# Kernel optimization log

Measured on AMD Instinct MI355X. Metric: run time of the kernel, lower is better.

The kernel has to match this reference:

```python
import jax, jax.numpy as jnp
import numpy as np

N = 50000          # points
K = 16             # neighbors per query (n_max)
M = N * K          # ragged pair count
DIM = 96
HEADS = 6
HEAD_DIM = DIM // HEADS
WINDOW = 4.0
QUANT = 0.25
QGL = int(WINDOW / QUANT)   # quant_grid_length = 16
SCALE = HEAD_DIM ** -0.5


def setup_inputs() -> dict:
    key = jax.random.key(0)
    ks = jax.random.split(key, 10)
    feats = jax.random.normal(ks[0], (N, DIM), dtype=jnp.float32)
    xyz = jax.random.uniform(ks[1], (N, 3), dtype=jnp.float32) * 8.0
    index_0 = jnp.repeat(jnp.arange(N, dtype=jnp.int32), K)            # sorted query ids
    index_1 = jax.random.randint(ks[2], (M,), 0, N, dtype=jnp.int32)   # neighbor ids
    index_0_offsets = jnp.arange(N + 1, dtype=jnp.int32) * K
    W_qkv = jax.random.normal(ks[3], (DIM, 3 * DIM), dtype=jnp.float32) * 0.02
    b_qkv = jnp.zeros((3 * DIM,), dtype=jnp.float32)
    table_q = jax.random.normal(ks[4], (4 * QGL, HEADS, HEAD_DIM, 3), dtype=jnp.float32) * 0.02
    table_k = jax.random.normal(ks[5], (4 * QGL, HEADS, HEAD_DIM, 3), dtype=jnp.float32) * 0.02
    table_v = jax.random.normal(ks[6], (4 * QGL, HEADS, HEAD_DIM, 3), dtype=jnp.float32) * 0.02
    W_proj = jax.random.normal(ks[7], (DIM, DIM), dtype=jnp.float32) * 0.02
    b_proj = jnp.zeros((DIM,), dtype=jnp.float32)
    return {
        "feats": feats, "xyz": xyz,
        "index_0": index_0, "index_0_offsets": index_0_offsets, "n_max": K,
        "index_1": index_1, "shift_size": jnp.float32(0.0),
        "W_qkv": W_qkv, "b_qkv": b_qkv,
        "table_q": table_q, "table_k": table_k, "table_v": table_v,
        "W_proj": W_proj, "b_proj": b_proj,
    }


def reference(feats, xyz, index_0, index_0_offsets, n_max, index_1, shift_size,
              W_qkv, b_qkv, table_q, table_k, table_v, W_proj, b_proj):
    n = feats.shape[0]
    # qkv projection -> (N, 3, H, HD)
    qkv = (feats @ W_qkv + b_qkv).reshape(n, 3, HEADS, HEAD_DIM)
    q = qkv[:, 0] * SCALE
    k = qkv[:, 1]
    v = qkv[:, 2]

    # step1: per-pair QK dot product (pointops.attention_step1_v2)
    qg = q[index_0]                      # (M, H, HD) gathered by query id
    kg = k[index_1]                      # (M, H, HD) gathered by neighbor id
    attn = jnp.einsum('mhd,mhd->mh', qg, kg)   # (M, H)

    # quantized relative positions
    xyz_quant = jnp.floor(((xyz - xyz.min(axis=0) + shift_size) % WINDOW) / QUANT)
    rel = xyz_quant[index_0] - xyz_quant[index_1]       # (M, 3)
    rel_idx = (rel + (QGL - 1)).astype(jnp.int32)       # map_func, in [0, 2*QGL-2]

    # relative position bias (pointops.dot_prod_with_idx_v3: query + key tables)
    bias = jnp.zeros_like(attn)
    for c in range(3):   # fixed 3 coordinate axes
        tq = table_q[rel_idx[:, c], :, :, c]            # (M, H, HD)
        tk = table_k[rel_idx[:, c], :, :, c]
        bias = bias + jnp.einsum('mhd,mhd->mh', qg, tq) + jnp.einsum('mhd,mhd->mh', kg, tk)
    attn = attn + bias

    # scatter softmax over index_0 segments
    seg_max = jax.ops.segment_max(attn, index_0, num_segments=n)
    e = jnp.exp(attn - seg_max[index_0])
    denom = jax.ops.segment_sum(e, index_0, num_segments=n)
    sm = e / denom[index_0]                              # (M, H)

    # step2 with relative position value (pointops.attention_step2_with_rel_pos_value_v2)
    vg = v[index_1]                                      # (M, H, HD)
    for c in range(3):
        vg = vg + table_v[rel_idx[:, c], :, :, c]
    x = jax.ops.segment_sum(sm[:, :, None] * vg, index_0, num_segments=n)  # (N, H, HD)
    x = x.reshape(n, DIM)
    return x @ W_proj + b_proj
```

## Files before the change

### kernel.cpp

```cpp
#include <hip/hip_runtime.h>
#include <hip/hip_fp16.h>
#include <math.h>

#define FLT_BIG 3.402823466e38f
typedef unsigned int uint;
typedef unsigned short ushort;
typedef __attribute__((ext_vector_type(8))) _Float16 half8;
typedef __attribute__((ext_vector_type(4))) float floatx4;

__device__ inline ushort f2h(float f) {
    return __half_as_ushort(__float2half(f));
}
__device__ inline float dot2(uint a, uint b, float c) {
    float d;
    asm("v_dot2_f32_f16 %0, %1, %2, %3" : "=v"(d) : "v"(a), "v"(b), "v"(c));
    return d;
}
template <int CTRL>
__device__ inline float dppf(float x) {
    return __int_as_float(__builtin_amdgcn_update_dpp(
        __float_as_int(x), __float_as_int(x), CTRL, 0xF, 0xF, true));
}

__global__ void prep_min_kernel(const float* __restrict__ W_qkv,
                                const float* __restrict__ W_proj,
                                const float* __restrict__ tq, const float* __restrict__ tk,
                                const float* __restrict__ tv,
                                const float* __restrict__ xyz,
                                ushort* __restrict__ wtqkv, ushort* __restrict__ wtproj,
                                ushort* __restrict__ rq, ushort* __restrict__ rk,
                                ushort* __restrict__ rv, float* mn, int n) {
    int tid = blockIdx.x * 256 + threadIdx.x;
    if (tid < 18432) {
        int c = tid / 6144, rem = tid - c * 6144;
        int idx = rem / 96, hd = rem - idx * 96;
        int src = (idx * 96 + hd) * 3 + c;
        rq[tid] = f2h(tq[src]);
        rk[tid] = f2h(tk[src]);
        rv[tid] = f2h(tv[src]);
    }
    if (tid < 27648) {
        int j = tid / 96, d = tid - j * 96;
        wtqkv[tid] = f2h(W_qkv[d * 288 + j]);
    }
    if (tid < 9216) {
        int j = tid / 96, d = tid - j * 96;
        wtproj[tid] = f2h(W_proj[d * 96 + j]);
    }
    float m0 = FLT_BIG, m1 = FLT_BIG, m2 = FLT_BIG;
    for (int i = tid; i < n; i += gridDim.x * 256) {
        m0 = fminf(m0, xyz[3 * i + 0]);
        m1 = fminf(m1, xyz[3 * i + 1]);
        m2 = fminf(m2, xyz[3 * i + 2]);
    }
#pragma unroll
    for (int off = 32; off > 0; off >>= 1) {
        m0 = fminf(m0, __shfl_down(m0, off));
        m1 = fminf(m1, __shfl_down(m1, off));
        m2 = fminf(m2, __shfl_down(m2, off));
    }
    if ((threadIdx.x & 63) == 0) {
        atomicMin((int*)&mn[0], __float_as_int(m0));
        atomicMin((int*)&mn[1], __float_as_int(m1));
        atomicMin((int*)&mn[2], __float_as_int(m2));
    }
}

__global__ __launch_bounds__(384) void qkv_mfma_kernel(
    const float* __restrict__ A, const ushort* __restrict__ WT,
    const float* __restrict__ bias, uint4* __restrict__ qout4,
    uint4* __restrict__ kvout4, const float* __restrict__ xyz,
    const float* __restrict__ mn, const float* __restrict__ shiftp,
    uint* __restrict__ xq, int n) {
    __shared__ ushort Ash[64 * 104];
    __shared__ ushort lds[6][32 * 112];
    const int t = threadIdx.x;
    const int row0 = blockIdx.x * 64;

    if (t < 64) {
        int rp = row0 + t;
        if (rp < n) {
            float shift = shiftp[0];
            float q0 = floorf(fmodf(xyz[3 * rp + 0] - mn[0] + shift, 4.0f) * 4.0f);
            float q1 = floorf(fmodf(xyz[3 * rp + 1] - mn[1] + shift, 4.0f) * 4.0f);
            float q2 = floorf(fmodf(xyz[3 * rp + 2] - mn[2] + shift, 4.0f) * 4.0f);
            xq[rp] = (uint)(int)q0 | ((uint)(int)q1 << 8) | ((uint)(int)q2 << 16);
        }
    }

    const float4* A4 = (const float4*)A;
#pragma unroll
    for (int j = 0; j < 4; j++) {
        int idx = t + j * 384;
        int row = idx / 24, c4 = idx - row * 24;
        int gr = row0 + row; if (gr > n - 1) gr = n - 1;
        float4 v = A4[(size_t)gr * 24 + c4];
        uint2 pk;
        pk.x = (uint)f2h(v.x) | ((uint)f2h(v.y) << 16);
        pk.y = (uint)f2h(v.z) | ((uint)f2h(v.w) << 16);
        *(uint2*)&Ash[row * 104 + c4 * 4] = pk;
    }
    __syncthreads();

    const int wave = t >> 6, lane = t & 63;
    const int ch = wave >> 1, rg = wave & 1;
    const int m = lane & 15, q = lane >> 4;
    const int wrow0 = row0 + rg * 32;

    const ushort* wbase = WT + ((size_t)ch * 96 + m) * 96 + q * 8;

    floatx4 acc[2][6];
#pragma unroll
    for (int g = 0; g < 2; g++)
#pragma unroll
        for (int ct = 0; ct < 6; ct++) acc[g][ct] = (floatx4){0.f, 0.f, 0.f, 0.f};

#pragma unroll
    for (int kk4 = 0; kk4 < 24; kk4 += 8) {
        half8 a0 = *(const half8*)&Ash[(rg * 32 + m) * 104 + (kk4 + q * 2) * 4];
        half8 a1 = *(const half8*)&Ash[(rg * 32 + 16 + m) * 104 + (kk4 + q * 2) * 4];
#pragma unroll
        for (int ct = 0; ct < 6; ct++) {
            half8 b = *(const half8*)(wbase + ct * 16 * 96 + kk4 * 4);
            acc[0][ct] = __builtin_amdgcn_mfma_f32_16x16x32_f16(a0, b, acc[0][ct], 0, 0, 0);
            acc[1][ct] = __builtin_amdgcn_mfma_f32_16x16x32_f16(a1, b, acc[1][ct], 0, 0, 0);
        }
    }

    ushort* L = lds[wave];
    const float sc = (ch == 0) ? 0.25f : 1.0f;
#pragma unroll
    for (int g = 0; g < 2; g++)
#pragma unroll
        for (int ct = 0; ct < 6; ct++) {
            float bv = bias[ch * 96 + ct * 16 + m];
#pragma unroll
            for (int r = 0; r < 4; r++) {
                int rowl = g * 16 + q * 4 + r;
                L[rowl * 112 + ct * 16 + m] = f2h((acc[g][ct][r] + bv) * sc);
            }
        }
    const int strideU4 = (ch == 0) ? 12 : 24;
    const int offU4 = (ch == 2) ? 12 : 0;
    uint4* dst = (ch == 0) ? qout4 : kvout4;
#pragma unroll
    for (int i = 0; i < 6; i++) {
        int idx = i * 64 + lane;
        int rowl = idx / 12, u4 = idx - rowl * 12;
        int grow = wrow0 + rowl;
        if (grow < n) {
            uint4 val = *(const uint4*)(L + rowl * 112 + u4 * 8);
            dst[(size_t)grow * strideU4 + offU4 + u4] = val;
        }
    }
}

#define ATTN_NB 256
#define ATTN_B 8
#define QPITCH 208
#define VPITCH 192
#define KOFF 39936
#define VOFF 79872
#define XOFF 116736
#define XPITCH 104
__global__ __launch_bounds__(768) void attn_proj_kernel(
    const ushort* __restrict__ qh, const ushort* __restrict__ kv,
    const uint* __restrict__ xq, const int* __restrict__ index_1,
    const ushort* __restrict__ rq, const ushort* __restrict__ rk,
    const ushort* __restrict__ rv, const ushort* __restrict__ wtproj,
    const float* __restrict__ b_proj, float* __restrict__ out, int n) {
    __shared__ __align__(16) char Lb[158336];

    const int t = threadIdx.x, b = blockIdx.x;
    const int pt = t / 96, tp = t - pt * 96;
    const int h = tp >> 4, e = tp & 15;

    const int stride = ATTN_NB * ATTN_B;
    const int iters = (n + stride - 1) / stride;

    int pA, jdA; uint xqpA;
    auto PREF_A = [&](int it) {
        pA = (it * ATTN_NB + b) * ATTN_B + pt;
        int pc = pA < n ? pA : n - 1;
        jdA = index_1[(size_t)pc * 16 + e];
        xqpA = xq[pc];
    };
    int p, jd; uint xqp, xqj;
    uint4 ka, kb, va, vb, qa, qb;
    auto PREF_B = [&]() {
        p = pA; jd = jdA; xqp = xqpA;
        int pc = p < n ? p : n - 1;
        const ushort* row = kv + (size_t)jd * 192;
        ka = *(const uint4*)(row + h * 16);
        kb = *(const uint4*)(row + h * 16 + 8);
        va = *(const uint4*)(row + 96 + h * 16);
        vb = *(const uint4*)(row + 96 + h * 16 + 8);
        const ushort* qrow = qh + (size_t)pc * 96 + h * 16;
        qa = *(const uint4*)qrow;
        qb = *(const uint4*)(qrow + 8);
        xqj = xq[jd];
    };
    PREF_A(0); PREF_B(); PREF_A(1);

#pragma unroll
    for (int j = 0; j < 9; j++) {
        const int tbl = j / 3;
        const uint4* src = (tbl == 0) ? (const uint4*)rq
                         : (tbl == 1) ? (const uint4*)rk : (const uint4*)rv;
        int rem = t + (j % 3) * 768;
        int ROW = rem / 12, slot = rem - ROW * 12;
        uint4 val = src[rem];
        const int base = (tbl == 0) ? 0 : (tbl == 1) ? KOFF : VOFF;
        const int pitch = (tbl == 2) ? VPITCH : QPITCH;
        *(uint4*)(Lb + base + ROW * pitch + slot * 16) = val;
    }
    __syncthreads();

    auto LD2Q = [&](const char* base, int R, uint4& A, uint4& B) {
        const char* rb = base + R * QPITCH + h * 32;
        A = *(const uint4*)rb;
        B = *(const uint4*)(rb + 16);
    };
    auto F2 = [](const uint4& u, int i) -> float2 {
        return __half22float2(((const __half2*)&u)[i]);
    };

    const bool b3 = (e & 8) != 0, b2 = (e & 4) != 0;
    const bool b1 = (e & 2) != 0, b0 = (e & 1) != 0;

    for (int it = 0; it < iters; it++) {
        const int i0 = (int)(xqp & 255u) - (int)(xqj & 255u) + 15;
        const int i1 = (int)((xqp >> 8) & 255u) - (int)((xqj >> 8) & 255u) + 15;
        const int i2 = (int)((xqp >> 16) & 255u) - (int)((xqj >> 16) & 255u) + 15;

        float f[16];
#pragma unroll
        for (int i = 0; i < 4; i++) {
            float2 lo = F2(va, i), hi = F2(vb, i);
            f[2 * i] = lo.x; f[2 * i + 1] = lo.y;
            f[8 + 2 * i] = hi.x; f[8 + 2 * i + 1] = hi.y;
        }

        float a;
        {
            float x0 = dot2(qa.x, ka.x, 0.f), x1 = dot2(qa.y, ka.y, 0.f);
            x0 = dot2(qa.z, ka.z, x0); x1 = dot2(qa.w, ka.w, x1);
            x0 = dot2(qb.x, kb.x, x0); x1 = dot2(qb.y, kb.y, x1);
            x0 = dot2(qb.z, kb.z, x0); x1 = dot2(qb.w, kb.w, x1);
            float bias = 0.f;
#define BIAS_C(ROW)                                                            \
            {                                                                  \
                uint4 ta, tb, ua, ub;                                          \
                LD2Q(Lb, (ROW), ta, tb);                                       \
                LD2Q(Lb + KOFF, (ROW), ua, ub);                                \
                float u = dot2(qa.x, ta.x, 0.f), w = dot2(ka.x, ua.x, 0.f);    \
                u = dot2(qa.y, ta.y, u); w = dot2(ka.y, ua.y, w);              \
                u = dot2(qa.z, ta.z, u); w = dot2(ka.z, ua.z, w);              \
                u = dot2(qa.w, ta.w, u); w = dot2(ka.w, ua.w, w);              \
                u = dot2(qb.x, tb.x, u); w = dot2(kb.x, ub.x, w);              \
                u = dot2(qb.y, tb.y, u); w = dot2(kb.y, ub.y, w);              \
                u = dot2(qb.z, tb.z, u); w = dot2(kb.z, ub.z, w);              \
                u = dot2(qb.w, tb.w, u); w = dot2(kb.w, ub.w, w);              \
                bias += u + w;                                                 \
            }
            BIAS_C(i0)
            BIAS_C(64 + i1)
            BIAS_C(128 + i2)
#undef BIAS_C
            a = x0 + x1 + bias;
        }

        if (it + 1 < iters) { PREF_B(); PREF_A(it + 2); }

        {
            uint4 t0a, t0b, t1a, t1b, t2a, t2b;
            {
                const char* rb = Lb + VOFF + i0 * VPITCH + h * 32;
                t0a = *(const uint4*)rb; t0b = *(const uint4*)(rb + 16);
            }
            {
                const char* rb = Lb + VOFF + (64 + i1) * VPITCH + h * 32;
                t1a = *(const uint4*)rb; t1b = *(const uint4*)(rb + 16);
            }
            {
                const char* rb = Lb + VOFF + (128 + i2) * VPITCH + h * 32;
                t2a = *(const uint4*)rb; t2b = *(const uint4*)(rb + 16);
            }
#pragma unroll
            for (int i = 0; i < 4; i++) {
                float2 a0 = F2(t0a, i), a1 = F2(t1a, i), a2 = F2(t2a, i);
                f[2 * i]     += a0.x + a1.x + a2.x;
                f[2 * i + 1] += a0.y + a1.y + a2.y;
                float2 c0 = F2(t0b, i), c1 = F2(t1b, i), c2 = F2(t2b, i);
                f[8 + 2 * i]     += c0.x + c1.x + c2.x;
                f[8 + 2 * i + 1] += c0.y + c1.y + c2.y;
            }
        }

        float wgt;
        {
            float mx = a;
            mx = fmaxf(mx, dppf<0x128>(mx));
            mx = fmaxf(mx, dppf<0x124>(mx));
            mx = fmaxf(mx, dppf<0x122>(mx));
            mx = fmaxf(mx, dppf<0x121>(mx));
            float ex = __expf(a - mx);
            float sum = ex;
            sum += dppf<0x128>(sum);
            sum += dppf<0x124>(sum);
            sum += dppf<0x122>(sum);
            sum += dppf<0x121>(sum);
            wgt = ex * __builtin_amdgcn_rcpf(sum);
        }

        float P[16];
#pragma unroll
        for (int c = 0; c < 16; c++) P[c] = wgt * f[c];
        float A8[8];
#pragma unroll
        for (int j = 0; j < 8; j++) {
            float kp = b3 ? P[j + 8] : P[j];
            float sd = b3 ? P[j] : P[j + 8];
            A8[j] = kp + dppf<0x140>(sd);
        }
        float B4[4];
#pragma unroll
        for (int j = 0; j < 4; j++) {
            float kp = b2 ? A8[j + 4] : A8[j];
            float sd = b2 ? A8[j] : A8[j + 4];
            B4[j] = kp + dppf<0x141>(sd);
        }
        float C2[2];
#pragma unroll
        for (int j = 0; j < 2; j++) {
            float kp = b1 ? B4[j + 2] : B4[j];
            float sd = b1 ? B4[j] : B4[j + 2];
            C2[j] = kp + dppf<0x4E>(sd);
        }
        {
            float kp = b0 ? C2[1] : C2[0];
            float sd = b0 ? C2[0] : C2[1];
            float xres = kp + dppf<0xB1>(sd);
            *(ushort*)(Lb + XOFF + (it * ATTN_B + pt) * (XPITCH * 2) + tp * 2) =
                f2h(xres);
        }
    }
    __syncthreads();

    {
        const int wave = t >> 6, lane = t & 63;
        const int m = lane & 15, q = lane >> 4;
        const int row0l = wave * 32;
        const int nloc = iters * ATTN_B;
        if (row0l < nloc) {
            const ushort* X = (const ushort*)(Lb + XOFF);
            const ushort* wbase = wtproj + (size_t)m * 96 + q * 8;
            int r0 = row0l + m;      if (r0 > nloc - 1) r0 = nloc - 1;
            int r1 = row0l + 16 + m; if (r1 > nloc - 1) r1 = nloc - 1;
            floatx4 acc[2][6];
#pragma unroll
            for (int g = 0; g < 2; g++)
#pragma unroll
                for (int ct = 0; ct < 6; ct++) acc[g][ct] = (floatx4){0.f, 0.f, 0.f, 0.f};
#pragma unroll
            for (int kk = 0; kk < 96; kk += 32) {
                half8 a0 = *(const half8*)(X + r0 * XPITCH + q * 8 + kk);
                half8 a1 = *(const half8*)(X + r1 * XPITCH + q * 8 + kk);
#pragma unroll
                for (int ct = 0; ct < 6; ct++) {
                    half8 bb = *(const half8*)(wbase + ct * 16 * 96 + kk);
                    acc[0][ct] = __builtin_amdgcn_mfma_f32_16x16x32_f16(a0, bb, acc[0][ct], 0, 0, 0);
                    acc[1][ct] = __builtin_amdgcn_mfma_f32_16x16x32_f16(a1, bb, acc[1][ct], 0, 0, 0);
                }
            }
#pragma unroll
            for (int g = 0; g < 2; g++)
#pragma unroll
                for (int ct = 0; ct < 6; ct++) {
                    int col = ct * 16 + m;
                    float bv = b_proj[col];
#pragma unroll
                    for (int r = 0; r < 4; r++) {
                        int lr = row0l + g * 16 + q * 4 + r;
                        if (lr < nloc) {
                            int grow = (lr >> 3) * stride + b * ATTN_B + (lr & 7);
                            if (grow < n)
                                out[(size_t)grow * 96 + col] = acc[g][ct][r] + bv;
                        }
                    }
                }
        }
    }
}

extern "C" void kernel_launch(void* const* d_in, const int* in_sizes, int n_in,
                              void* d_out, int out_size, void* d_ws, size_t ws_size,
                              hipStream_t stream) {
    const float* feats   = (const float*)d_in[0];
    const float* xyz     = (const float*)d_in[1];
    const int*   index_1 = (const int*)d_in[5];
    const float* shiftp  = (const float*)d_in[6];
    const float* W_qkv   = (const float*)d_in[7];
    const float* b_qkv   = (const float*)d_in[8];
    const float* table_q = (const float*)d_in[9];
    const float* table_k = (const float*)d_in[10];
    const float* table_v = (const float*)d_in[11];
    const float* W_proj  = (const float*)d_in[12];
    const float* b_proj  = (const float*)d_in[13];
    float* out = (float*)d_out;

    const int n = in_sizes[0] / 96;

    float* w = (float*)d_ws;
    float*  mn     = w;
    ushort* qbf    = (ushort*)(w + 16);
    ushort* kvbuf  = qbf + (size_t)n * 96;
    ushort* wtqkv  = kvbuf + (size_t)n * 192;
    ushort* wtproj = wtqkv + 27648;
    ushort* rq     = wtproj + 9216;
    ushort* rk     = rq + 18432;
    ushort* rv     = rk + 18432;
    uint*   xqv    = (uint*)(rv + 18432);

    hipMemsetAsync(mn, 0x7F, 3 * sizeof(float), stream);
    prep_min_kernel<<<108, 256, 0, stream>>>(W_qkv, W_proj, table_q, table_k,
                                             table_v, xyz, wtqkv, wtproj,
                                             rq, rk, rv, mn, n);
    qkv_mfma_kernel<<<(n + 63) / 64, 384, 0, stream>>>(feats, wtqkv, b_qkv,
                                                       (uint4*)qbf, (uint4*)kvbuf,
                                                       xyz, mn, shiftp, xqv, n);
    attn_proj_kernel<<<ATTN_NB, 768, 0, stream>>>(qbf, kvbuf, xqv, index_1,
                                                  rq, rk, rv, wtproj, b_proj,
                                                  out, n);
}
```

Measured before the change: 200.7 us.

## Process two points per thread-group per iteration and sum value tables in half2

Each 96-thread group now handles two query points per loop iteration (16 points per block iteration instead of 8), doubling the number of independent gathers and computations in flight per thread. This is meant to expose more memory-level and instruction-level parallelism to hide gather latency, with half the iterations. The three relative-position value table rows are also summed in packed fp16 before conversion, which cuts conversion and add work but loses a little precision. The cost is higher register pressure, and the shared X buffer grows with more rows per block.

```diff
diff --git a/kernel.cpp b/kernel.cpp
--- a/kernel.cpp
+++ b/kernel.cpp
@@ -156,51 +156,52 @@
 }
 
 #define ATTN_NB 256
-#define ATTN_B 8
+#define PPB 16
 #define QPITCH 208
 #define VPITCH 192
 #define KOFF 39936
 #define VOFF 79872
 #define XOFF 116736
 #define XPITCH 104
-__global__ __launch_bounds__(768) void attn_proj_kernel(
+__global__ __launch_bounds__(768, 3) void attn_proj_kernel(
     const ushort* __restrict__ qh, const ushort* __restrict__ kv,
     const uint* __restrict__ xq, const int* __restrict__ index_1,
     const ushort* __restrict__ rq, const ushort* __restrict__ rk,
     const ushort* __restrict__ rv, const ushort* __restrict__ wtproj,
     const float* __restrict__ b_proj, float* __restrict__ out, int n) {
-    __shared__ __align__(16) char Lb[158336];
+    __shared__ __align__(16) char Lb[160000];
 
     const int t = threadIdx.x, b = blockIdx.x;
     const int pt = t / 96, tp = t - pt * 96;
     const int h = tp >> 4, e = tp & 15;
 
-    const int stride = ATTN_NB * ATTN_B;
+    const int stride = ATTN_NB * PPB;
     const int iters = (n + stride - 1) / stride;
 
-    int pA, jdA; uint xqpA;
-    auto PREF_A = [&](int it) {
-        pA = (it * ATTN_NB + b) * ATTN_B + pt;
-        int pc = pA < n ? pA : n - 1;
-        jdA = index_1[(size_t)pc * 16 + e];
-        xqpA = xq[pc];
+    int pA[2], jdA[2]; uint xqpA[2];
+    auto PREF_A = [&](int it, int u) {
+        pA[u] = (it * ATTN_NB + b) * PPB + u * 8 + pt;
+        int pc = pA[u] < n ? pA[u] : n - 1;
+        jdA[u] = index_1[(size_t)pc * 16 + e];
+        xqpA[u] = xq[pc];
     };
-    int p, jd; uint xqp, xqj;
-    uint4 ka, kb, va, vb, qa, qb;
-    auto PREF_B = [&]() {
-        p = pA; jd = jdA; xqp = xqpA;
-        int pc = p < n ? p : n - 1;
-        const ushort* row = kv + (size_t)jd * 192;
-        ka = *(const uint4*)(row + h * 16);
-        kb = *(const uint4*)(row + h * 16 + 8);
-        va = *(const uint4*)(row + 96 + h * 16);
-        vb = *(const uint4*)(row + 96 + h * 16 + 8);
+    int p[2], jd[2]; uint xqp[2], xqj[2];
+    uint4 ka[2], kb[2], va[2], vb[2], qa[2], qb[2];
+    auto PREF_B = [&](int u) {
+        p[u] = pA[u]; jd[u] = jdA[u]; xqp[u] = xqpA[u];
+        int pc = p[u] < n ? p[u] : n - 1;
+        const ushort* row = kv + (size_t)jd[u] * 192;
+        ka[u] = *(const uint4*)(row + h * 16);
+        kb[u] = *(const uint4*)(row + h * 16 + 8);
+        va[u] = *(const uint4*)(row + 96 + h * 16);
+        vb[u] = *(const uint4*)(row + 96 + h * 16 + 8);
         const ushort* qrow = qh + (size_t)pc * 96 + h * 16;
-        qa = *(const uint4*)qrow;
-        qb = *(const uint4*)(qrow + 8);
-        xqj = xq[jd];
+        qa[u] = *(const uint4*)qrow;
+        qb[u] = *(const uint4*)(qrow + 8);
+        xqj[u] = xq[jd[u]];
     };
-    PREF_A(0); PREF_B(); PREF_A(1);
+    PREF_A(0, 0); PREF_A(0, 1); PREF_B(0); PREF_B(1);
+    PREF_A(1, 0); PREF_A(1, 1);
 
 #pragma unroll
     for (int j = 0; j < 9; j++) {
@@ -224,125 +225,146 @@
     auto F2 = [](const uint4& u, int i) -> float2 {
         return __half22float2(((const __half2*)&u)[i]);
     };
-
-    const bool b3 = (e & 8) != 0, b2 = (e & 4) != 0;
-    const bool b1 = (e & 2) != 0, b0 = (e & 1) != 0;
+    auto H2 = [](const uint4& u, int i) -> __half2 {
+        return ((const __half2*)&u)[i];
+    };
+
+    const bool e3 = (e & 8) != 0, e2 = (e & 4) != 0;
+    const bool e1 = (e & 2) != 0, e0 = (e & 1) != 0;
 
     for (int it = 0; it < iters; it++) {
-        const int i0 = (int)(xqp & 255u) - (int)(xqj & 255u) + 15;
-        const int i1 = (int)((xqp >> 8) & 255u) - (int)((xqj >> 8) & 255u) + 15;
-        const int i2 = (int)((xqp >> 16) & 255u) - (int)((xqj >> 16) & 255u) + 15;
-
-        float f[16];
-#pragma unroll
-        for (int i = 0; i < 4; i++) {
-            float2 lo = F2(va, i), hi = F2(vb, i);
-            f[2 * i] = lo.x; f[2 * i + 1] = lo.y;
-            f[8 + 2 * i] = hi.x; f[8 + 2 * i + 1] = hi.y;
-        }
-
-        float a;
-        {
-            float x0 = dot2(qa.x, ka.x, 0.f), x1 = dot2(qa.y, ka.y, 0.f);
-            x0 = dot2(qa.z, ka.z, x0); x1 = dot2(qa.w, ka.w, x1);
-            x0 = dot2(qb.x, kb.x, x0); x1 = dot2(qb.y, kb.y, x1);
-            x0 = dot2(qb.z, kb.z, x0); x1 = dot2(qb.w, kb.w, x1);
+        int i0[2], i1[2], i2[2];
+#pragma unroll
+        for (int u = 0; u < 2; u++) {
+            i0[u] = (int)(xqp[u] & 255u) - (int)(xqj[u] & 255u) + 15;
+            i1[u] = (int)((xqp[u] >> 8) & 255u) - (int)((xqj[u] >> 8) & 255u) + 15;
+            i2[u] = (int)((xqp[u] >> 16) & 255u) - (int)((xqj[u] >> 16) & 255u) + 15;
+        }
+
+        float f[2][16];
+#pragma unroll
+        for (int u = 0; u < 2; u++)
+#pragma unroll
+            for (int i = 0; i < 4; i++) {
+                float2 lo = F2(va[u], i), hi = F2(vb[u], i);
+                f[u][2 * i] = lo.x; f[u][2 * i + 1] = lo.y;
+                f[u][8 + 2 * i] = hi.x; f[u][8 + 2 * i + 1] = hi.y;
+            }
+
+        float a[2];
+#pragma unroll
+        for (int u = 0; u < 2; u++) {
+            float x0 = dot2(qa[u].x, ka[u].x, 0.f), x1 = dot2(qa[u].y, ka[u].y, 0.f);
+            x0 = dot2(qa[u].z, ka[u].z, x0); x1 = dot2(qa[u].w, ka[u].w, x1);
+            x0 = dot2(qb[u].x, kb[u].x, x0); x1 = dot2(qb[u].y, kb[u].y, x1);
+            x0 = dot2(qb[u].z, kb[u].z, x0); x1 = dot2(qb[u].w, kb[u].w, x1);
             float bias = 0.f;
 #define BIAS_C(ROW)                                                            \
             {                                                                  \
                 uint4 ta, tb, ua, ub;                                          \
                 LD2Q(Lb, (ROW), ta, tb);                                       \
                 LD2Q(Lb + KOFF, (ROW), ua, ub);                                \
-                float u = dot2(qa.x, ta.x, 0.f), w = dot2(ka.x, ua.x, 0.f);    \
-                u = dot2(qa.y, ta.y, u); w = dot2(ka.y, ua.y, w);              \
-                u = dot2(qa.z, ta.z, u); w = dot2(ka.z, ua.z, w);              \
-                u = dot2(qa.w, ta.w, u); w = dot2(ka.w, ua.w, w);              \
-                u = dot2(qb.x, tb.x, u); w = dot2(kb.x, ub.x, w);              \
-                u = dot2(qb.y, tb.y, u); w = dot2(kb.y, ub.y, w);              \
-                u = dot2(qb.z, tb.z, u); w = dot2(kb.z, ub.z, w);              \
-                u = dot2(qb.w, tb.w, u); w = dot2(kb.w, ub.w, w);              \
-                bias += u + w;                                                 \
-            }
-            BIAS_C(i0)
-            BIAS_C(64 + i1)
-            BIAS_C(128 + i2)
+                float uu = dot2(qa[u].x, ta.x, 0.f), w = dot2(ka[u].x, ua.x, 0.f);\
+                uu = dot2(qa[u].y, ta.y, uu); w = dot2(ka[u].y, ua.y, w);      \
+                uu = dot2(qa[u].z, ta.z, uu); w = dot2(ka[u].z, ua.z, w);      \
+                uu = dot2(qa[u].w, ta.w, uu); w = dot2(ka[u].w, ua.w, w);      \
+                uu = dot2(qb[u].x, tb.x, uu); w = dot2(kb[u].x, ub.x, w);      \
+                uu = dot2(qb[u].y, tb.y, uu); w = dot2(kb[u].y, ub.y, w);      \
+                uu = dot2(qb[u].z, tb.z, uu); w = dot2(kb[u].z, ub.z, w);      \
+                uu = dot2(qb[u].w, tb.w, uu); w = dot2(kb[u].w, ub.w, w);      \
+                bias += uu + w;                                                \
+            }
+            BIAS_C(i0[u])
+            BIAS_C(64 + i1[u])
+            BIAS_C(128 + i2[u])
 #undef BIAS_C
-            a = x0 + x1 + bias;
-        }
-
-        if (it + 1 < iters) { PREF_B(); PREF_A(it + 2); }
-
-        {
+            a[u] = x0 + x1 + bias;
+        }
+
+        const int op0 = p[0], op1 = p[1]; (void)op0; (void)op1;
+        if (it + 1 < iters) {
+            PREF_B(0); PREF_B(1);
+            PREF_A(it + 2, 0); PREF_A(it + 2, 1);
+        }
+
+#pragma unroll
+        for (int u = 0; u < 2; u++) {
             uint4 t0a, t0b, t1a, t1b, t2a, t2b;
             {
-                const char* rb = Lb + VOFF + i0 * VPITCH + h * 32;
+                const char* rb = Lb + VOFF + i0[u] * VPITCH + h * 32;
                 t0a = *(const uint4*)rb; t0b = *(const uint4*)(rb + 16);
             }
             {
-                const char* rb = Lb + VOFF + (64 + i1) * VPITCH + h * 32;
+                const char* rb = Lb + VOFF + (64 + i1[u]) * VPITCH + h * 32;
                 t1a = *(const uint4*)rb; t1b = *(const uint4*)(rb + 16);
             }
             {
-                const char* rb = Lb + VOFF + (128 + i2) * VPITCH + h * 32;
+                const char* rb = Lb + VOFF + (128 + i2[u]) * VPITCH + h * 32;
                 t2a = *(const uint4*)rb; t2b = *(const uint4*)(rb + 16);
             }
 #pragma unroll
             for (int i = 0; i < 4; i++) {
-                float2 a0 = F2(t0a, i), a1 = F2(t1a, i), a2 = F2(t2a, i);
-                f[2 * i]     += a0.x + a1.x + a2.x;
-                f[2 * i + 1] += a0.y + a1.y + a2.y;
-                float2 c0 = F2(t0b, i), c1 = F2(t1b, i), c2 = F2(t2b, i);
-                f[8 + 2 * i]     += c0.x + c1.x + c2.x;
-                f[8 + 2 * i + 1] += c0.y + c1.y + c2.y;
-            }
-        }
-
-        float wgt;
-        {
-            float mx = a;
+                __half2 sa = H2(t0a, i) + H2(t1a, i) + H2(t2a, i);
+                __half2 sb = H2(t0b, i) + H2(t1b, i) + H2(t2b, i);
+                float2 fa = __half22float2(sa), fb = __half22float2(sb);
+                f[u][2 * i]     += fa.x;
+                f[u][2 * i + 1] += fa.y;
+                f[u][8 + 2 * i]     += fb.x;
+                f[u][8 + 2 * i + 1] += fb.y;
+            }
+        }
+
+        float wgt[2];
+#pragma unroll
+        for (int u = 0; u < 2; u++) {
+            float mx = a[u];
             mx = fmaxf(mx, dppf<0x128>(mx));
             mx = fmaxf(mx, dppf<0x124>(mx));
             mx = fmaxf(mx, dppf<0x122>(mx));
             mx = fmaxf(mx, dppf<0x121>(mx));
-            float ex = __expf(a - mx);
+            float ex = __expf(a[u] - mx);
             float sum = ex;
             sum += dppf<0x128>(sum);
             sum += dppf<0x124>(sum);
             sum += dppf<0x122>(sum);
             sum += dppf<0x121>(sum);
-            wgt = ex * __builtin_amdgcn_rcpf(sum);
-        }
-
-        float P[16];
-#pragma unroll
-        for (int c = 0; c < 16; c++) P[c] = wgt * f[c];
-        float A8[8];
-#pragma unroll
-        for (int j = 0; j < 8; j++) {
-            float kp = b3 ? P[j + 8] : P[j];
-            float sd = b3 ? P[j] : P[j + 8];
-            A8[j] = kp + dppf<0x140>(sd);
-        }
-        float B4[4];
-#pragma unroll
-        for (int j = 0; j < 4; j++) {
-            float kp = b2 ? A8[j + 4] : A8[j];
-            float sd = b2 ? A8[j] : A8[j + 4];
-            B4[j] = kp + dppf<0x141>(sd);
-        }
-        float C2[2];
-#pragma unroll
-        for (int j = 0; j < 2; j++) {
-            float kp = b1 ? B4[j + 2] : B4[j];
-            float sd = b1 ? B4[j] : B4[j + 2];
-            C2[j] = kp + dppf<0x4E>(sd);
-        }
-        {
-            float kp = b0 ? C2[1] : C2[0];
-            float sd = b0 ? C2[0] : C2[1];
-            float xres = kp + dppf<0xB1>(sd);
-            *(ushort*)(Lb + XOFF + (it * ATTN_B + pt) * (XPITCH * 2) + tp * 2) =
-                f2h(xres);
+            wgt[u] = ex * __builtin_amdgcn_rcpf(sum);
+        }
+
+#pragma unroll
+        for (int u = 0; u < 2; u++) {
+            float P[16];
+#pragma unroll
+            for (int c = 0; c < 16; c++) P[c] = wgt[u] * f[u][c];
+            float A8[8];
+#pragma unroll
+            for (int j = 0; j < 8; j++) {
+                float kp = e3 ? P[j + 8] : P[j];
+                float sd = e3 ? P[j] : P[j + 8];
+                A8[j] = kp + dppf<0x140>(sd);
+            }
+            float B4[4];
+#pragma unroll
+            for (int j = 0; j < 4; j++) {
+                float kp = e2 ? A8[j + 4] : A8[j];
+                float sd = e2 ? A8[j] : A8[j + 4];
+                B4[j] = kp + dppf<0x141>(sd);
+            }
+            float C2[2];
+#pragma unroll
+            for (int j = 0; j < 2; j++) {
+                float kp = e1 ? B4[j + 2] : B4[j];
+                float sd = e1 ? B4[j] : B4[j + 2];
+                C2[j] = kp + dppf<0x4E>(sd);
+            }
+            {
+                float kp = e0 ? C2[1] : C2[0];
+                float sd = e0 ? C2[0] : C2[1];
+                float xres = kp + dppf<0xB1>(sd);
+                *(ushort*)(Lb + XOFF +
+                           (it * PPB + u * 8 + pt) * (XPITCH * 2) + tp * 2) =
+                    f2h(xres);
+            }
         }
     }
     __syncthreads();
@@ -351,7 +373,7 @@
         const int wave = t >> 6, lane = t & 63;
         const int m = lane & 15, q = lane >> 4;
         const int row0l = wave * 32;
-        const int nloc = iters * ATTN_B;
+        const int nloc = iters * PPB;
         if (row0l < nloc) {
             const ushort* X = (const ushort*)(Lb + XOFF);
             const ushort* wbase = wtproj + (size_t)m * 96 + q * 8;
@@ -383,7 +405,7 @@
                     for (int r = 0; r < 4; r++) {
                         int lr = row0l + g * 16 + q * 4 + r;
                         if (lr < nloc) {
-                            int grow = (lr >> 3) * stride + b * ATTN_B + (lr & 7);
+                            int grow = (lr >> 4) * stride + b * PPB + (lr & 15);
                             if (grow < n)
                                 out[(size_t)grow * 96 + col] = acc[g][ct][r] + bv;
                         }
```

Measured after the change: 204.3 us. No clear change (+1.8%).
